# Kernel tuning notes

Hardware: AMD Instinct MI355X
Metric: run time of the kernel (lower is better)

The kernel has to match this reference:

```python
import jax, jax.numpy as jnp
import numpy as np
from jax import lax

L, H, NUM_CONVS, KSIZE = 8192, 128, 4, 7
EPS = 1e-5


def _pos_encoding(length, dim, dtype):
    pos = jnp.arange(length, dtype=jnp.float32)[:, None]
    i = jnp.arange(dim, dtype=jnp.float32)[None, :]
    angle = pos / jnp.power(10000.0, (2.0 * jnp.floor(i / 2.0)) / dim)
    pe = jnp.where((jnp.arange(dim) % 2 == 0)[None, :], jnp.sin(angle), jnp.cos(angle))
    return pe.astype(dtype)


def _layer_norm(x):
    mu = jnp.mean(x, axis=-1, keepdims=True)
    var = jnp.mean(jnp.square(x - mu), axis=-1, keepdims=True)
    return (x - mu) * lax.rsqrt(var + EPS)


def _conv1d_same(x, w, b):
    # x: [L, H]; w: [H_out, H_in, K]; b: [H_out]. SAME padding over sequence.
    lhs = x.T[None]  # [1, H, L]
    out = lax.conv_general_dilated(lhs, w, window_strides=(1,), padding='SAME',
                                   dimension_numbers=('NCH', 'OIH', 'NCH'))
    return (out[0] + b[:, None]).T  # [L, H]


def setup_inputs() -> dict:
    key = jax.random.key(0)
    ks = jax.random.split(key, 12)
    s = 0.02
    return {
        'x': jax.random.normal(ks[0], (L, H), jnp.float32),
        'conv_w': jax.random.normal(ks[1], (NUM_CONVS, H, H, KSIZE), jnp.float32) * s,
        'conv_b': jax.random.normal(ks[2], (NUM_CONVS, H), jnp.float32) * s,
        'Wq': jax.random.normal(ks[3], (H, H), jnp.float32) * s,
        'bq': jax.random.normal(ks[4], (H,), jnp.float32) * s,
        'Wk': jax.random.normal(ks[5], (H, H), jnp.float32) * s,
        'bk': jax.random.normal(ks[6], (H,), jnp.float32) * s,
        'Wv': jax.random.normal(ks[7], (H, H), jnp.float32) * s,
        'bv': jax.random.normal(ks[8], (H,), jnp.float32) * s,
        'Wff': jax.random.normal(ks[9], (H, H), jnp.float32) * s,
        'bff': jax.random.normal(ks[10], (H,), jnp.float32) * s,
    }


def reference(x, conv_w, conv_b, Wq, bq, Wk, bk, Wv, bv, Wff, bff):
    h = x + _pos_encoding(x.shape[0], x.shape[1], x.dtype)
    # conv stack: LN -> conv -> residual, repeated num_convs times
    for i in range(NUM_CONVS):
        residual = h
        h = _conv1d_same(_layer_norm(h), conv_w[i], conv_b[i]) + residual
    # self-attention (single-head as written in the source)
    residual = h
    n = _layer_norm(h)
    q = n @ Wq.T + bq
    k = n @ Wk.T + bk
    v = n @ Wv.T + bv
    scale = 1.0 / jnp.sqrt(jnp.asarray(H, h.dtype))
    attn = jax.nn.softmax((q @ k.T) * scale, axis=-1)  # [L, L]
    h = attn @ v + residual
    # feed-forward
    residual = h
    h = jax.nn.relu(_layer_norm(h) @ Wff.T + bff) + residual
    return h
```

## Files before the change

### kernel.cpp

```cpp
#include <hip/hip_runtime.h>

#define LL 8192
#define HH 128

typedef __attribute__((ext_vector_type(8))) short short8v;
typedef __attribute__((ext_vector_type(4))) short short4v;
typedef __attribute__((ext_vector_type(4))) float f32x4;

__device__ inline short f2bf(float f) {
    union { float f; unsigned u; } x; x.f = f;
    unsigned r = (x.u + 0x7fffu + ((x.u >> 16) & 1u)) >> 16;
    return (short)r;
}
__device__ inline float bf2f(short s) {
    union { unsigned u; float f; } x; x.u = ((unsigned)(unsigned short)s) << 16;
    return x.f;
}

__device__ inline unsigned ln_pack(const float* rowF, int lane) {
    float2 xv = *(const float2*)&rowF[lane * 2];
    float s = xv.x + xv.y, s2 = xv.x * xv.x + xv.y * xv.y;
#pragma unroll
    for (int off = 32; off >= 1; off >>= 1) {
        s  += __shfl_xor(s,  off, 64);
        s2 += __shfl_xor(s2, off, 64);
    }
    float mu = s * (1.f / 128.f);
    float var = s2 * (1.f / 128.f) - mu * mu;
    float rstd = rsqrtf(var + 1e-5f);
    unsigned lo = (unsigned short)f2bf((xv.x - mu) * rstd);
    unsigned hi = (unsigned short)f2bf((xv.y - mu) * rstd);
    return lo | (hi << 16);
}

__global__ __launch_bounds__(256) void repack_all(const float* __restrict__ w,
                                                  const float* __restrict__ Wq,
                                                  const float* __restrict__ Wk,
                                                  const float* __restrict__ Wv,
                                                  const float* __restrict__ bq,
                                                  const float* __restrict__ bk,
                                                  const float* __restrict__ bv,
                                                  const float* __restrict__ Wff,
                                                  short* __restrict__ wkb,
                                                  short* __restrict__ wqkvb,
                                                  float* __restrict__ b3,
                                                  short* __restrict__ wffb) {
    const float qs = 0.08838834764831845f;
    int idx = blockIdx.x * 256 + threadIdx.x;
    if (idx < 458752) {
        int k = idx % 7;
        int t = idx / 7;
        int i = t % HH; t /= HH;
        int o = t % HH;
        int lay = t / HH;
        wkb[((lay * 7 + k) * HH + o) * HH + i] = f2bf(w[idx]);
    } else {
        int j = idx - 458752;
        if (j < 49152) {
            int t = j >> 14, r = j & 16383;
            float v = (t == 0) ? Wq[r] * qs : (t == 1) ? Wk[r] : Wv[r];
            wqkvb[j] = f2bf(v);
        } else if (j < 49536) {
            int jj = j - 49152;
            b3[jj] = (jj < 128) ? bq[jj] * qs : (jj < 256) ? bk[jj - 128] : bv[jj - 256];
        } else if (j < 65920) {
            int jj = j - 49536;
            wffb[jj] = f2bf(Wff[jj]);
        }
    }
}

__global__ __launch_bounds__(256) void conv4qkv_kernel(const float* __restrict__ x,
                                                       const short* __restrict__ wkb,
                                                       const float* __restrict__ conv_b,
                                                       const short* __restrict__ wqkvb,
                                                       const float* __restrict__ b3,
                                                       float* __restrict__ hB,
                                                       short* __restrict__ qb,
                                                       short* __restrict__ kb,
                                                       short* __restrict__ vt) {
    __shared__ float sF[48][132];
    __shared__ short sA[54][136];
    __shared__ short sT[4][32][17];
    int tid = threadIdx.x;
    int w = tid >> 6, lane = tid & 63;
    int l15 = lane & 15, quad = lane >> 4;
    int m0 = blockIdx.x * 16;
    int c0 = w * 32;

    for (int idx = tid; idx < 48 * 32; idx += 256) {
        int r = idx >> 5, c4 = (idx & 31) << 2;
        int g = m0 - 16 + r;
        float4 val = make_float4(0.f, 0.f, 0.f, 0.f);
        if (g >= 0 && g < LL) {
            val = *(const float4*)&x[g * HH + c4];
#pragma unroll
            for (int j = 0; j < 4; j++) {
                int i = c4 + j;
                float e = (float)(i & ~1) / 128.f;
                float ang = (float)g / powf(10000.f, e);
                float pe = (i & 1) ? cosf(ang) : sinf(ang);
                ((float*)&val)[j] += pe;
            }
        }
        *(float4*)&sF[r][c4] = val;
    }
    for (int idx = tid; idx < 6 * 68; idx += 256) {
        int rr = idx / 68, cc = idx % 68;
        int row = (rr < 3) ? rr : 48 + rr;
        ((unsigned*)&sA[row][0])[cc] = 0u;
    }

    for (int lay = 0; lay < 4; lay++) {
        __syncthreads();
#pragma unroll
        for (int rr = 0; rr < 12; rr++) {
            int row = rr * 4 + w;
            int g = m0 - 16 + row;
            unsigned packed = ln_pack(&sF[row][0], lane);
            if (g < 0 || g >= LL) packed = 0u;
            ((unsigned*)&sA[row + 3][0])[lane] = packed;
        }
        __syncthreads();
        f32x4 acc[3][2];
#pragma unroll
        for (int mt = 0; mt < 3; mt++) { acc[mt][0] = (f32x4)(0.f); acc[mt][1] = (f32x4)(0.f); }
        const short* wl = wkb + lay * 7 * HH * HH;
        for (int k = 0; k < 7; k++) {
            const short* b0 = wl + (k * HH + c0 + l15) * HH;
            const short* b1 = b0 + 16 * HH;
#pragma unroll
            for (int ks = 0; ks < 4; ks++) {
                short8v bf0 = *(const short8v*)&b0[ks * 32 + quad * 8];
                short8v bf1 = *(const short8v*)&b1[ks * 32 + quad * 8];
#pragma unroll
                for (int mt = 0; mt < 3; mt++) {
                    short8v af = *(const short8v*)&sA[mt * 16 + l15 + k][ks * 32 + quad * 8];
                    acc[mt][0] = __builtin_amdgcn_mfma_f32_16x16x32_bf16(af, bf0, acc[mt][0], 0, 0, 0);
                    acc[mt][1] = __builtin_amdgcn_mfma_f32_16x16x32_bf16(af, bf1, acc[mt][1], 0, 0, 0);
                }
            }
        }
        float bb0 = conv_b[lay * HH + c0 + l15], bb1 = conv_b[lay * HH + c0 + 16 + l15];
#pragma unroll
        for (int mt = 0; mt < 3; mt++)
#pragma unroll
            for (int r = 0; r < 4; r++) {
                int row = mt * 16 + quad * 4 + r;
                sF[row][c0 + l15]      += acc[mt][0][r] + bb0;
                sF[row][c0 + 16 + l15] += acc[mt][1][r] + bb1;
            }
    }
    __syncthreads();
    for (int idx = tid; idx < 16 * 32; idx += 256) {
        int r = idx >> 5, c4 = (idx & 31) << 2;
        *(float4*)&hB[(m0 + r) * HH + c4] = *(const float4*)&sF[16 + r][c4];
    }
#pragma unroll
    for (int rr = 0; rr < 4; rr++) {
        int row = rr * 4 + w;
        ((unsigned*)&sA[row][0])[lane] = ln_pack(&sF[16 + row][0], lane);
    }
    __syncthreads();
    short8v af4[4];
#pragma unroll
    for (int ks = 0; ks < 4; ks++)
        af4[ks] = *(const short8v*)&sA[l15][ks * 32 + quad * 8];

    for (int t = 0; t < 3; t++) {
        f32x4 acc0 = (f32x4)(0.f), acc1 = (f32x4)(0.f);
        const short* b0 = wqkvb + (t * 128 + c0 + l15) * HH;
        const short* b1 = b0 + 16 * HH;
#pragma unroll
        for (int ks = 0; ks < 4; ks++) {
            short8v bf0 = *(const short8v*)&b0[ks * 32 + quad * 8];
            short8v bf1 = *(const short8v*)&b1[ks * 32 + quad * 8];
            acc0 = __builtin_amdgcn_mfma_f32_16x16x32_bf16(af4[ks], bf0, acc0, 0, 0, 0);
            acc1 = __builtin_amdgcn_mfma_f32_16x16x32_bf16(af4[ks], bf1, acc1, 0, 0, 0);
        }
        float bb0 = b3[t * 128 + c0 + l15], bb1 = b3[t * 128 + c0 + 16 + l15];
        if (t < 2) {
            short* o = (t == 0) ? qb : kb;
#pragma unroll
            for (int r = 0; r < 4; r++) {
                int lr = m0 + quad * 4 + r;
                o[lr * HH + c0 + l15]      = f2bf(acc0[r] + bb0);
                o[lr * HH + c0 + 16 + l15] = f2bf(acc1[r] + bb1);
            }
        } else {
#pragma unroll
            for (int r = 0; r < 4; r++) {
                sT[w][l15][quad * 4 + r]      = f2bf(acc0[r] + bb0);
                sT[w][16 + l15][quad * 4 + r] = f2bf(acc1[r] + bb1);
            }
            asm volatile("s_waitcnt lgkmcnt(0)" ::: "memory");
#pragma unroll
            for (int cc = 0; cc < 8; cc++) {
                int col = cc * 4 + quad;
                vt[(c0 + col) * LL + m0 + l15] = sT[w][col][l15];
            }
        }
    }
}

#define FBN 64

__global__ __launch_bounds__(256, 2) void flash_mfma_kernel(const short* __restrict__ qs,
                                                            const short* __restrict__ ksrc,
                                                            const short* __restrict__ vsrc,
                                                            short* __restrict__ PO,
                                                            float* __restrict__ Pl,
                                                            int segrows) {
    __shared__ short sK[16 * 64 * 8];
    __shared__ short sV[16 * 64 * 8];
    __shared__ short sP[4][32][72];

    const int tid = threadIdx.x;
    const int w = tid >> 6, lane = tid & 63;
    const int l15 = lane & 15, quad = lane >> 4;
    const int m0 = blockIdx.x * 128;
    const int seg = blockIdx.y;
    const int jbeg = seg * segrows;
    const int nchunk = segrows >> 6;

    const int vdt_base = (w >> 1);
    const int vks2 = w & 1;

    short8v qf[2][4];
#pragma unroll
    for (int mt = 0; mt < 2; mt++)
#pragma unroll
        for (int ks = 0; ks < 4; ks++)
            qf[mt][ks] = *(const short8v*)&qs[(m0 + w * 32 + mt * 16 + l15) * HH + ks * 32 + quad * 8];

    float l_r[2][4] = {{0.f, 0.f, 0.f, 0.f}, {0.f, 0.f, 0.f, 0.f}};
    f32x4 o_acc[2][8];
#pragma unroll
    for (int mt = 0; mt < 2; mt++)
#pragma unroll
        for (int dt = 0; dt < 8; dt++) o_acc[mt][dt] = (f32x4)(0.f);

    short8v kr[4], vr[4];
#pragma unroll
    for (int r = 0; r < 4; r++) {
        kr[r] = *(const short8v*)&ksrc[(jbeg + r * 16 + l15) * HH + w * 32 + quad * 8];
        vr[r] = *(const short8v*)&vsrc[((2 * r + vdt_base) * 16 + l15) * LL + jbeg + vks2 * 32 + quad * 8];
    }

    for (int c = 0; c < nchunk; c++) {
        __syncthreads();
#pragma unroll
        for (int r = 0; r < 4; r++) {
            *(short8v*)&sK[((w + 4 * r) * 64 + lane) * 8] = kr[r];
            *(short8v*)&sV[((w + 4 * r) * 64 + lane) * 8] = vr[r];
        }
        __syncthreads();
        if (c + 1 < nchunk) {
            const int j1 = jbeg + (c + 1) * FBN;
#pragma unroll
            for (int r = 0; r < 4; r++) {
                kr[r] = *(const short8v*)&ksrc[(j1 + r * 16 + l15) * HH + w * 32 + quad * 8];
                vr[r] = *(const short8v*)&vsrc[((2 * r + vdt_base) * 16 + l15) * LL + j1 + vks2 * 32 + quad * 8];
            }
        }
        f32x4 s_acc[2][4];
#pragma unroll
        for (int mt = 0; mt < 2; mt++)
#pragma unroll
            for (int nt = 0; nt < 4; nt++) s_acc[mt][nt] = (f32x4)(0.f);
#pragma unroll
        for (int nt = 0; nt < 4; nt++)
#pragma unroll
            for (int ks = 0; ks < 4; ks++) {
                short8v kf = *(const short8v*)&sK[((nt * 4 + ks) * 64 + lane) * 8];
                s_acc[0][nt] = __builtin_amdgcn_mfma_f32_16x16x32_bf16(qf[0][ks], kf, s_acc[0][nt], 0, 0, 0);
                s_acc[1][nt] = __builtin_amdgcn_mfma_f32_16x16x32_bf16(qf[1][ks], kf, s_acc[1][nt], 0, 0, 0);
            }
#pragma unroll
        for (int mt = 0; mt < 2; mt++)
#pragma unroll
            for (int nt = 0; nt < 4; nt++)
#pragma unroll
                for (int r = 0; r < 4; r++) {
                    float p = __expf(fminf(s_acc[mt][nt][r], 30.f));
                    l_r[mt][r] += p;
                    union { float f; unsigned u; } cv; cv.f = p;
                    sP[w][mt * 16 + quad * 4 + r][nt * 16 + l15] = (short)(cv.u >> 16);
                }
        asm volatile("s_waitcnt lgkmcnt(0)" ::: "memory");
#pragma unroll
        for (int ks2 = 0; ks2 < 2; ks2++) {
            short8v pf0 = *(const short8v*)&sP[w][l15][ks2 * 32 + quad * 8];
            short8v pf1 = *(const short8v*)&sP[w][16 + l15][ks2 * 32 + quad * 8];
#pragma unroll
            for (int dt = 0; dt < 8; dt++) {
                short8v vf = *(const short8v*)&sV[((dt * 2 + ks2) * 64 + lane) * 8];
                o_acc[0][dt] = __builtin_amdgcn_mfma_f32_16x16x32_bf16(pf0, vf, o_acc[0][dt], 0, 0, 0);
                o_acc[1][dt] = __builtin_amdgcn_mfma_f32_16x16x32_bf16(pf1, vf, o_acc[1][dt], 0, 0, 0);
            }
        }
    }
#pragma unroll
    for (int mt = 0; mt < 2; mt++)
#pragma unroll
        for (int r = 0; r < 4; r++) {
            float v = l_r[mt][r];
            v += __shfl_xor(v, 1, 64);
            v += __shfl_xor(v, 2, 64);
            v += __shfl_xor(v, 4, 64);
            v += __shfl_xor(v, 8, 64);
            if (l15 == 0)
                Pl[seg * LL + m0 + w * 32 + mt * 16 + quad * 4 + r] = v;
        }
#pragma unroll
    for (int mt = 0; mt < 2; mt++)
#pragma unroll
        for (int dt = 0; dt < 8; dt++)
#pragma unroll
            for (int r = 0; r < 4; r++)
                PO[(size_t)seg * LL * HH + (m0 + w * 32 + mt * 16 + quad * 4 + r) * HH + dt * 16 + l15] =
                    f2bf(o_acc[mt][dt][r]);
}

__global__ __launch_bounds__(256) void ff_kernel(const float* __restrict__ hin,
                                                 const short* __restrict__ PO,
                                                 const float* __restrict__ Pl,
                                                 const short* __restrict__ wffb,
                                                 const float* __restrict__ bff,
                                                 float* __restrict__ out,
                                                 int nsplit) {
    __shared__ float sF[16][132];
    __shared__ short sA[16][136];
    __shared__ float sLi[16];
    int tid = threadIdx.x;
    int w = tid >> 6, lane = tid & 63;
    int l15 = lane & 15, quad = lane >> 4;
    int m0 = blockIdx.x * 16;

    if (tid < 16) {
        float s = 0.f;
        for (int seg = 0; seg < nsplit; seg++) s += Pl[seg * LL + m0 + tid];
        sLi[tid] = 1.f / s;
    }
    __syncthreads();
    for (int idx = tid; idx < 16 * 32; idx += 256) {
        int r = idx >> 5, c4 = (idx & 31) << 2;
        float4 hv = *(const float4*)&hin[(m0 + r) * HH + c4];
        float s0 = 0.f, s1 = 0.f, s2 = 0.f, s3 = 0.f;
        for (int seg = 0; seg < nsplit; seg++) {
            short4v pv = *(const short4v*)&PO[(size_t)seg * LL * HH + (m0 + r) * HH + c4];
            s0 += bf2f(pv[0]); s1 += bf2f(pv[1]); s2 += bf2f(pv[2]); s3 += bf2f(pv[3]);
        }
        float li = sLi[r];
        *(float4*)&sF[r][c4] = make_float4(hv.x + s0 * li, hv.y + s1 * li,
                                           hv.z + s2 * li, hv.w + s3 * li);
    }
    __syncthreads();
#pragma unroll
    for (int rr = 0; rr < 4; rr++) {
        int row = rr * 4 + w;
        ((unsigned*)&sA[row][0])[lane] = ln_pack(&sF[row][0], lane);
    }
    __syncthreads();
    int c0 = w * 32;
    f32x4 acc0 = (f32x4)(0.f), acc1 = (f32x4)(0.f);
    const short* b0 = wffb + (c0 + l15) * HH;
    const short* b1 = b0 + 16 * HH;
#pragma unroll
    for (int ks = 0; ks < 4; ks++) {
        short8v af = *(const short8v*)&sA[l15][ks * 32 + quad * 8];
        short8v bf0 = *(const short8v*)&b0[ks * 32 + quad * 8];
        short8v bf1 = *(const short8v*)&b1[ks * 32 + quad * 8];
        acc0 = __builtin_amdgcn_mfma_f32_16x16x32_bf16(af, bf0, acc0, 0, 0, 0);
        acc1 = __builtin_amdgcn_mfma_f32_16x16x32_bf16(af, bf1, acc1, 0, 0, 0);
    }
    float bb0 = bff[c0 + l15], bb1 = bff[c0 + 16 + l15];
#pragma unroll
    for (int r = 0; r < 4; r++) {
        int lr = quad * 4 + r;
        out[(m0 + lr) * HH + c0 + l15]      = fmaxf(acc0[r] + bb0, 0.f) + sF[lr][c0 + l15];
        out[(m0 + lr) * HH + c0 + 16 + l15] = fmaxf(acc1[r] + bb1, 0.f) + sF[lr][c0 + 16 + l15];
    }
}

extern "C" void kernel_launch(void* const* d_in, const int* in_sizes, int n_in,
                              void* d_out, int out_size, void* d_ws, size_t ws_size,
                              hipStream_t stream) {
    const float* x      = (const float*)d_in[0];
    const float* conv_w = (const float*)d_in[1];
    const float* conv_b = (const float*)d_in[2];
    const float* Wq = (const float*)d_in[3];
    const float* bq = (const float*)d_in[4];
    const float* Wk = (const float*)d_in[5];
    const float* bk = (const float*)d_in[6];
    const float* Wv = (const float*)d_in[7];
    const float* bv = (const float*)d_in[8];
    const float* Wff = (const float*)d_in[9];
    const float* bff = (const float*)d_in[10];
    float* out = (float*)d_out;

    char* ws = (char*)d_ws;
    const size_t MB = 1u << 20;
    float* hB   = (float*)(ws);
    short* qb   = (short*)(ws + 4 * MB);
    short* kb   = (short*)(ws + 6 * MB);
    short* vt   = (short*)(ws + 8 * MB);
    float* Pl   = (float*)(ws + 10 * MB);
    short* wffb = (short*)(ws + 10 * MB + 524288);
    short* PO   = (short*)(ws + 10 * MB + 524288 + 32768);
    short* wkb   = (short*)(ws + 16 * MB);
    short* wqkvb = (short*)(ws + 17 * MB);
    float* b3    = (float*)(ws + 17 * MB + 131072);

    int nsplit = (ws_size >= (size_t)44 * MB) ? 16 : 8;
    int segrows = LL / nsplit;

    repack_all<<<2050, 256, 0, stream>>>(conv_w, Wq, Wk, Wv, bq, bk, bv, Wff,
                                         wkb, wqkvb, b3, wffb);
    conv4qkv_kernel<<<LL / 16, 256, 0, stream>>>(x, wkb, conv_b, wqkvb, b3,
                                                 hB, qb, kb, vt);
    flash_mfma_kernel<<<dim3(LL / 128, nsplit), 256, 0, stream>>>(qb, kb, vt, PO, Pl, segrows);
    ff_kernel<<<LL / 16, 256, 0, stream>>>(hB, PO, Pl, wffb, bff, out, nsplit);
}
```

Measured before the change: 217.3 us.

## Split fused conv stack into per-layer kernels to drop halo recompute

The single fused conv+QKV kernel, which recomputed a 48-row halo for every 16-row output tile, is replaced by separate kernels. A positional-encoding+LayerNorm kernel runs first, then four per-layer conv kernels that ping-pong zero-padded bf16 normalized activations through global memory, then a standalone QKV projection kernel. This removes the threefold redundant conv MFMA work and the in-block serial layer chain, at the cost of extra kernel launches and global-memory round trips for the residual stream and normalized activations. The repack kernel now also zeroes the padding rows of the ping-pong buffers.

```diff
diff --git a/kernel.cpp b/kernel.cpp
--- a/kernel.cpp
+++ b/kernel.cpp
@@ -44,7 +44,9 @@
                                                   short* __restrict__ wkb,
                                                   short* __restrict__ wqkvb,
                                                   float* __restrict__ b3,
-                                                  short* __restrict__ wffb) {
+                                                  short* __restrict__ wffb,
+                                                  unsigned* __restrict__ nbA_u,
+                                                  unsigned* __restrict__ nbB_u) {
     const float qs = 0.08838834764831845f;
     int idx = blockIdx.x * 256 + threadIdx.x;
     if (idx < 458752) {
@@ -64,23 +66,97 @@
             int jj = j - 49152;
             b3[jj] = (jj < 128) ? bq[jj] * qs : (jj < 256) ? bk[jj - 128] : bv[jj - 256];
         } else if (j < 65920) {
-            int jj = j - 49536;
-            wffb[jj] = f2bf(Wff[jj]);
-        }
-    }
-}
-
-__global__ __launch_bounds__(256) void conv4qkv_kernel(const float* __restrict__ x,
-                                                       const short* __restrict__ wkb,
-                                                       const float* __restrict__ conv_b,
-                                                       const short* __restrict__ wqkvb,
-                                                       const float* __restrict__ b3,
-                                                       float* __restrict__ hB,
-                                                       short* __restrict__ qb,
-                                                       short* __restrict__ kb,
-                                                       short* __restrict__ vt) {
-    __shared__ float sF[48][132];
-    __shared__ short sA[54][136];
+            wffb[j - 49536] = f2bf(Wff[j - 49536]);
+        } else if (j < 65920 + 2048) {
+            int p = j - 65920;
+            int u = p & 511, which = p >> 9;
+            unsigned* base = (which < 2) ? nbA_u : nbB_u;
+            base[(which & 1) ? (524800 + u) : u] = 0u;
+        }
+    }
+}
+
+__global__ __launch_bounds__(256) void pos_ln_kernel(const float* __restrict__ x,
+                                                     float* __restrict__ h,
+                                                     short* __restrict__ nbp) {
+    int wave = threadIdx.x >> 6, lane = threadIdx.x & 63;
+    int row = blockIdx.x * 4 + wave;
+    int i0 = lane * 2;
+    float e = (float)i0 * (1.f / 128.f);
+    float denom = powf(10000.f, e);
+    float ang = (float)row / denom;
+    float sv = sinf(ang), cv = cosf(ang);
+    float2 xv = *(const float2*)&x[row * HH + i0];
+    float h0 = xv.x + sv, h1 = xv.y + cv;
+    *(float2*)&h[row * HH + i0] = make_float2(h0, h1);
+    float s = h0 + h1, s2 = h0 * h0 + h1 * h1;
+#pragma unroll
+    for (int off = 32; off >= 1; off >>= 1) {
+        s  += __shfl_xor(s,  off, 64);
+        s2 += __shfl_xor(s2, off, 64);
+    }
+    float mu = s * (1.f / 128.f);
+    float var = s2 * (1.f / 128.f) - mu * mu;
+    float rstd = rsqrtf(var + 1e-5f);
+    unsigned lo = (unsigned short)f2bf((h0 - mu) * rstd);
+    unsigned hi = (unsigned short)f2bf((h1 - mu) * rstd);
+    ((unsigned*)&nbp[row * HH])[lane] = lo | (hi << 16);
+}
+
+__global__ __launch_bounds__(256) void conv_ln_kernel(const short* __restrict__ nbp_in,
+                                                      const short* __restrict__ wkl,
+                                                      const float* __restrict__ bias,
+                                                      float* __restrict__ h,
+                                                      short* __restrict__ nbp_out) {
+    __shared__ float sF[16][132];
+    int tid = threadIdx.x;
+    int w = tid >> 6, lane = tid & 63;
+    int l15 = lane & 15, quad = lane >> 4;
+    int m0 = blockIdx.x * 16;
+    int c0 = w * 32;
+
+    f32x4 acc0 = (f32x4)(0.f), acc1 = (f32x4)(0.f);
+#pragma unroll
+    for (int k = 0; k < 7; k++) {
+        const short* ar = nbp_in + (m0 + l15 + k - 3) * HH;
+        const short* b0 = wkl + (k * HH + c0 + l15) * HH;
+        const short* b1 = b0 + 16 * HH;
+#pragma unroll
+        for (int ks = 0; ks < 4; ks++) {
+            short8v af  = *(const short8v*)&ar[ks * 32 + quad * 8];
+            short8v bf0 = *(const short8v*)&b0[ks * 32 + quad * 8];
+            short8v bf1 = *(const short8v*)&b1[ks * 32 + quad * 8];
+            acc0 = __builtin_amdgcn_mfma_f32_16x16x32_bf16(af, bf0, acc0, 0, 0, 0);
+            acc1 = __builtin_amdgcn_mfma_f32_16x16x32_bf16(af, bf1, acc1, 0, 0, 0);
+        }
+    }
+    float bb0 = bias[c0 + l15], bb1 = bias[c0 + 16 + l15];
+#pragma unroll
+    for (int r = 0; r < 4; r++) {
+        int rowL = quad * 4 + r;
+        int g = (m0 + rowL) * HH;
+        float z0 = h[g + c0 + l15]      + acc0[r] + bb0;
+        float z1 = h[g + c0 + 16 + l15] + acc1[r] + bb1;
+        h[g + c0 + l15]      = z0;
+        h[g + c0 + 16 + l15] = z1;
+        sF[rowL][c0 + l15]      = z0;
+        sF[rowL][c0 + 16 + l15] = z1;
+    }
+    __syncthreads();
+#pragma unroll
+    for (int rr = 0; rr < 4; rr++) {
+        int rowL = w * 4 + rr;
+        unsigned packed = ln_pack(&sF[rowL][0], lane);
+        ((unsigned*)&nbp_out[(m0 + rowL) * HH])[lane] = packed;
+    }
+}
+
+__global__ __launch_bounds__(256) void qkv_kernel(const short* __restrict__ nbp,
+                                                  const short* __restrict__ wqkvb,
+                                                  const float* __restrict__ b3,
+                                                  short* __restrict__ qb,
+                                                  short* __restrict__ kb,
+                                                  short* __restrict__ vt) {
     __shared__ short sT[4][32][17];
     int tid = threadIdx.x;
     int w = tid >> 6, lane = tid & 63;
@@ -88,84 +164,10 @@
     int m0 = blockIdx.x * 16;
     int c0 = w * 32;
 
-    for (int idx = tid; idx < 48 * 32; idx += 256) {
-        int r = idx >> 5, c4 = (idx & 31) << 2;
-        int g = m0 - 16 + r;
-        float4 val = make_float4(0.f, 0.f, 0.f, 0.f);
-        if (g >= 0 && g < LL) {
-            val = *(const float4*)&x[g * HH + c4];
-#pragma unroll
-            for (int j = 0; j < 4; j++) {
-                int i = c4 + j;
-                float e = (float)(i & ~1) / 128.f;
-                float ang = (float)g / powf(10000.f, e);
-                float pe = (i & 1) ? cosf(ang) : sinf(ang);
-                ((float*)&val)[j] += pe;
-            }
-        }
-        *(float4*)&sF[r][c4] = val;
-    }
-    for (int idx = tid; idx < 6 * 68; idx += 256) {
-        int rr = idx / 68, cc = idx % 68;
-        int row = (rr < 3) ? rr : 48 + rr;
-        ((unsigned*)&sA[row][0])[cc] = 0u;
-    }
-
-    for (int lay = 0; lay < 4; lay++) {
-        __syncthreads();
-#pragma unroll
-        for (int rr = 0; rr < 12; rr++) {
-            int row = rr * 4 + w;
-            int g = m0 - 16 + row;
-            unsigned packed = ln_pack(&sF[row][0], lane);
-            if (g < 0 || g >= LL) packed = 0u;
-            ((unsigned*)&sA[row + 3][0])[lane] = packed;
-        }
-        __syncthreads();
-        f32x4 acc[3][2];
-#pragma unroll
-        for (int mt = 0; mt < 3; mt++) { acc[mt][0] = (f32x4)(0.f); acc[mt][1] = (f32x4)(0.f); }
-        const short* wl = wkb + lay * 7 * HH * HH;
-        for (int k = 0; k < 7; k++) {
-            const short* b0 = wl + (k * HH + c0 + l15) * HH;
-            const short* b1 = b0 + 16 * HH;
-#pragma unroll
-            for (int ks = 0; ks < 4; ks++) {
-                short8v bf0 = *(const short8v*)&b0[ks * 32 + quad * 8];
-                short8v bf1 = *(const short8v*)&b1[ks * 32 + quad * 8];
-#pragma unroll
-                for (int mt = 0; mt < 3; mt++) {
-                    short8v af = *(const short8v*)&sA[mt * 16 + l15 + k][ks * 32 + quad * 8];
-                    acc[mt][0] = __builtin_amdgcn_mfma_f32_16x16x32_bf16(af, bf0, acc[mt][0], 0, 0, 0);
-                    acc[mt][1] = __builtin_amdgcn_mfma_f32_16x16x32_bf16(af, bf1, acc[mt][1], 0, 0, 0);
-                }
-            }
-        }
-        float bb0 = conv_b[lay * HH + c0 + l15], bb1 = conv_b[lay * HH + c0 + 16 + l15];
-#pragma unroll
-        for (int mt = 0; mt < 3; mt++)
-#pragma unroll
-            for (int r = 0; r < 4; r++) {
-                int row = mt * 16 + quad * 4 + r;
-                sF[row][c0 + l15]      += acc[mt][0][r] + bb0;
-                sF[row][c0 + 16 + l15] += acc[mt][1][r] + bb1;
-            }
-    }
-    __syncthreads();
-    for (int idx = tid; idx < 16 * 32; idx += 256) {
-        int r = idx >> 5, c4 = (idx & 31) << 2;
-        *(float4*)&hB[(m0 + r) * HH + c4] = *(const float4*)&sF[16 + r][c4];
-    }
-#pragma unroll
-    for (int rr = 0; rr < 4; rr++) {
-        int row = rr * 4 + w;
-        ((unsigned*)&sA[row][0])[lane] = ln_pack(&sF[16 + row][0], lane);
-    }
-    __syncthreads();
     short8v af4[4];
 #pragma unroll
     for (int ks = 0; ks < 4; ks++)
-        af4[ks] = *(const short8v*)&sA[l15][ks * 32 + quad * 8];
+        af4[ks] = *(const short8v*)&nbp[(m0 + l15) * HH + ks * 32 + quad * 8];
 
     for (int t = 0; t < 3; t++) {
         f32x4 acc0 = (f32x4)(0.f), acc1 = (f32x4)(0.f);
@@ -401,24 +403,38 @@
 
     char* ws = (char*)d_ws;
     const size_t MB = 1u << 20;
-    float* hB   = (float*)(ws);
+    float* h    = (float*)(ws);
     short* qb   = (short*)(ws + 4 * MB);
     short* kb   = (short*)(ws + 6 * MB);
     short* vt   = (short*)(ws + 8 * MB);
     float* Pl   = (float*)(ws + 10 * MB);
     short* wffb = (short*)(ws + 10 * MB + 524288);
-    short* PO   = (short*)(ws + 10 * MB + 524288 + 32768);
-    short* wkb   = (short*)(ws + 16 * MB);
-    short* wqkvb = (short*)(ws + 17 * MB);
-    float* b3    = (float*)(ws + 17 * MB + 131072);
+    short* PO   = (short*)(ws + 11 * MB);
+    short* nbA_all = (short*)(ws + 11 * MB);
+    short* nbB_all = (short*)(ws + 11 * MB + 2621440);
+    short* wkb     = (short*)(ws + 16 * MB);
+    short* wqkvb   = (short*)(ws + 17 * MB);
+    float* b3      = (float*)(ws + 17 * MB + 131072);
+    short* nbA = nbA_all + 8 * HH;
+    short* nbB = nbB_all + 8 * HH;
 
     int nsplit = (ws_size >= (size_t)44 * MB) ? 16 : 8;
     int segrows = LL / nsplit;
 
-    repack_all<<<2050, 256, 0, stream>>>(conv_w, Wq, Wk, Wv, bq, bk, bv, Wff,
-                                         wkb, wqkvb, b3, wffb);
-    conv4qkv_kernel<<<LL / 16, 256, 0, stream>>>(x, wkb, conv_b, wqkvb, b3,
-                                                 hB, qb, kb, vt);
+    repack_all<<<2058, 256, 0, stream>>>(conv_w, Wq, Wk, Wv, bq, bk, bv, Wff,
+                                         wkb, wqkvb, b3, wffb,
+                                         (unsigned*)nbA_all, (unsigned*)nbB_all);
+    pos_ln_kernel<<<LL / 4, 256, 0, stream>>>(x, h, nbA);
+
+    const int KW = 7 * HH * HH;
+    conv_ln_kernel<<<LL / 16, 256, 0, stream>>>(nbA, wkb + 0 * KW, conv_b + 0 * HH, h, nbB);
+    conv_ln_kernel<<<LL / 16, 256, 0, stream>>>(nbB, wkb + 1 * KW, conv_b + 1 * HH, h, nbA);
+    conv_ln_kernel<<<LL / 16, 256, 0, stream>>>(nbA, wkb + 2 * KW, conv_b + 2 * HH, h, nbB);
+    conv_ln_kernel<<<LL / 16, 256, 0, stream>>>(nbB, wkb + 3 * KW, conv_b + 3 * HH, h, nbA);
+
+    qkv_kernel<<<LL / 16, 256, 0, stream>>>(nbA, wqkvb, b3, qb, kb, vt);
+
     flash_mfma_kernel<<<dim3(LL / 128, nsplit), 256, 0, stream>>>(qb, kb, vt, PO, Pl, segrows);
-    ff_kernel<<<LL / 16, 256, 0, stream>>>(hB, PO, Pl, wffb, bff, out, nsplit);
-}
+
+    ff_kernel<<<LL / 16, 256, 0, stream>>>(h, PO, Pl, wffb, bff, out, nsplit);
+}
```

New measurement: 254.9 us. 17.3% more time.
